# Optimization experiments

Measured on AMD Instinct MI355X. Metric: run time of the kernel, lower is better.

The kernel has to match this reference:

```python
import jax, jax.numpy as jnp
import numpy as np

IN_DIM = 512
C_OUT = IN_DIM // 8  # 64
B, H, W = 8, 128, 128


def setup_inputs() -> dict:
    key = jax.random.key(0)
    ks = jax.random.split(key, 6)
    x = jax.random.normal(ks[0], (B, IN_DIM, H, W), dtype=jnp.float32)
    # 1x1 conv weights stored as [out_ch, in_ch] matrices (kernel size 1)
    qkv_w = jax.random.normal(ks[1], (3 * C_OUT, IN_DIM), dtype=jnp.float32) * (1.0 / np.sqrt(IN_DIM))
    qkv_b = jax.random.normal(ks[2], (3 * C_OUT,), dtype=jnp.float32) * 0.01
    out_w = jax.random.normal(ks[3], (IN_DIM, C_OUT), dtype=jnp.float32) * (1.0 / np.sqrt(C_OUT))
    out_b = jax.random.normal(ks[4], (IN_DIM,), dtype=jnp.float32) * 0.01
    # gamma is init to 0 in torch; use a small nonzero value so both paths are exercised
    gamma = jnp.asarray(0.5, dtype=jnp.float32)
    return {"x": x, "qkv_w": qkv_w, "qkv_b": qkv_b, "out_w": out_w, "out_b": out_b, "gamma": gamma}


def reference(x, qkv_w, qkv_b, out_w, out_b, gamma):
    # qkv_conv: 1x1 conv == channel matmul
    qkv = jnp.einsum('bchw,oc->bohw', x, qkv_w) + qkv_b[None, :, None, None]
    q, k, v = jnp.split(qkv, 3, axis=1)  # each [B, C', H, W]

    # Horizontal branch: per column w, channel-channel attention contracting over H
    energy_h = jnp.einsum('bqhw,bkhw->bwqk', q, k)          # [B, W, C', C']
    attn_h = jax.nn.softmax(energy_h, axis=-1)
    out_h = jnp.einsum('bwqk,bkhw->bqhw', attn_h, v)        # [B, C', H, W]

    # Vertical branch: per row h, channel-channel attention contracting over W
    energy_v = jnp.einsum('bqhw,bkhw->bhqk', q, k)          # [B, H, C', C']
    attn_v = jax.nn.softmax(energy_v, axis=-1)
    out_v = jnp.einsum('bhqk,bkhw->bqhw', attn_v, v)        # [B, C', H, W]

    out = gamma * (out_h + out_v)
    out = jnp.einsum('bchw,oc->bohw', out, out_w) + out_b[None, :, None, None]
    return out + x
```

## Files before the change

kernel.cpp:

```cpp
#include <hip/hip_runtime.h>


typedef _Float16 f16;
typedef _Float16 f16x4 __attribute__((ext_vector_type(4)));
typedef _Float16 f16x8 __attribute__((ext_vector_type(8)));
typedef float f32x4 __attribute__((ext_vector_type(4)));

#define MFMA16(a, b, c) __builtin_amdgcn_mfma_f32_16x16x32_f16(a, b, c, 0, 0, 0)

constexpr int CIN = 512;
constexpr int COUT = 64;
constexpr int HW = 128;
constexpr int P = HW * HW;
constexpr int QKV_CH = 192;

__global__ __launch_bounds__(256) void qkv_gemm(
    const float* __restrict__ x, const float* __restrict__ w,
    const float* __restrict__ bias, f16* __restrict__ qkv)
{
  __shared__ __attribute__((aligned(16))) f16 Wl[QKV_CH * 40];
  __shared__ __attribute__((aligned(16))) f16 Xt[128 * 40];
  const int p0 = blockIdx.x * 128;
  const int b = blockIdx.y;
  const float* xb = x + (size_t)b * CIN * P;
  const int t = threadIdx.x;
  const int lane = t & 63, wv = t >> 6;
  const int quad = lane >> 4, l15 = lane & 15;
  const int wm = (wv >> 1) * 32, wn = (wv & 1) * 64;

  f32x4 acc[3][4][2] = {};
  for (int k0 = 0; k0 < CIN; k0 += 32) {
    for (int it = 0; it < 6; ++it) {
      int c = t + it * 256;
      int row = c >> 3, c4 = (c & 7) * 4;
      const float4 v = *(const float4*)(w + (size_t)row * CIN + k0 + c4);
      f16* d = &Wl[row * 40 + c4];
      d[0] = (f16)v.x; d[1] = (f16)v.y; d[2] = (f16)v.z; d[3] = (f16)v.w;
    }
    for (int it = 0; it < 4; ++it) {
      int c = t + it * 256;
      int kr = c >> 5, p4 = (c & 31) * 4;
      const float4 v = *(const float4*)(xb + (size_t)(k0 + kr) * P + p0 + p4);
      float vv[4] = {v.x, v.y, v.z, v.w};
#pragma unroll
      for (int j = 0; j < 4; ++j) {
        int p = p4 + j;
        int kc = kr ^ (((p >> 3) & 3) << 3);
        Xt[p * 40 + kc] = (f16)vv[j];
      }
    }
    __syncthreads();
    f16x8 xf[4];
#pragma unroll
    for (int ps = 0; ps < 4; ++ps) {
      int pr = wn + ps * 16 + l15;
      int kb = (quad * 8) ^ (((pr >> 3) & 3) << 3);
      xf[ps] = *(const f16x8*)&Xt[pr * 40 + kb];
    }
#pragma unroll
    for (int mt = 0; mt < 3; ++mt) {
      f16x8 wf[2];
#pragma unroll
      for (int ms = 0; ms < 2; ++ms)
        wf[ms] = *(const f16x8*)&Wl[(mt * 64 + wm + ms * 16 + l15) * 40 + quad * 8];
#pragma unroll
      for (int ps = 0; ps < 4; ++ps)
#pragma unroll
        for (int ms = 0; ms < 2; ++ms)
          acc[mt][ps][ms] = MFMA16(xf[ps], wf[ms], acc[mt][ps][ms]);
    }
    __syncthreads();
  }
  f16* ob = qkv + (size_t)b * QKV_CH * P;
#pragma unroll
  for (int mt = 0; mt < 3; ++mt) {
#pragma unroll
    for (int ms = 0; ms < 2; ++ms) {
      int m = mt * 64 + wm + ms * 16 + l15;
      float bi = bias[m];
#pragma unroll
      for (int ps = 0; ps < 4; ++ps) {
        int p = p0 + wn + ps * 16 + quad * 4;
        f16x4 tmp;
#pragma unroll
        for (int r = 0; r < 4; ++r) tmp[r] = (f16)(acc[mt][ps][ms][r] + bi);
        *(f16x4*)(ob + (size_t)m * P + p) = tmp;
      }
    }
  }
}

__global__ __launch_bounds__(256) void transpose_hw(
    const f16* __restrict__ in, f16* __restrict__ out)
{
  __shared__ __attribute__((aligned(16))) f16 T[64 * 72];
  const size_t plane = blockIdx.x;
  const int r0 = blockIdx.y * 64, c0 = blockIdx.z * 64;
  const f16* ip = in + plane * P;
  f16* op = out + plane * P;
  const int t = threadIdx.x;
  for (int it = 0; it < 2; ++it) {
    int c = t + it * 256;
    int row = c >> 3, c8 = (c & 7) * 8;
    *(f16x8*)&T[row * 72 + c8] =
        *(const f16x8*)(ip + (size_t)(r0 + row) * HW + c0 + c8);
  }
  __syncthreads();
  for (int it = 0; it < 2; ++it) {
    int c = t + it * 256;
    int wr = c >> 3, h8 = (c & 7) * 8;
    f16 tmp[8];
#pragma unroll
    for (int j = 0; j < 8; ++j) tmp[j] = T[(h8 + j) * 72 + wr];
    *(f16x8*)(op + (size_t)(c0 + wr) * HW + r0 + h8) = *(const f16x8*)tmp;
  }
}

__global__ __launch_bounds__(256) void cc_attn(
    const f16* __restrict__ qkvT, const f16* __restrict__ qkvN,
    f16* __restrict__ outT, f16* __restrict__ outN)
{
  __shared__ __attribute__((aligned(16))) f16 smem[64 * 136 * 2 + 128 * 72];
  f16* Ql = smem;
  f16* Kl = smem + 64 * 136;
  f16* Vt = smem + 2 * 64 * 136;
  f16* Al = smem;
  const int s = blockIdx.x, b = blockIdx.y;
  const f16* src = blockIdx.z ? qkvN : qkvT;
  f16* dst = blockIdx.z ? outN : outT;
  const f16* base = src + (size_t)b * QKV_CH * P + (size_t)s * HW;
  const int t = threadIdx.x;
  const int lane = t & 63, wv = t >> 6;
  const int quad = lane >> 4, l15 = lane & 15;

  for (int it = 0; it < 4; ++it) {
    int c = t + it * 256;
    int row = c >> 4, c8 = (c & 15) * 8;
    *(f16x8*)&Ql[row * 136 + c8] = *(const f16x8*)(base + (size_t)row * P + c8);
    *(f16x8*)&Kl[row * 136 + c8] =
        *(const f16x8*)(base + (size_t)(64 + row) * P + c8);
    f16x8 v = *(const f16x8*)(base + (size_t)(128 + row) * P + c8);
#pragma unroll
    for (int j = 0; j < 8; ++j) {
      int h = c8 + j;
      int kc = row ^ (((h >> 3) & 7) << 3);
      Vt[h * 72 + kc] = v[j];
    }
  }
  __syncthreads();

  const int m0 = wv * 16;
  f32x4 e[4] = {};
#pragma unroll
  for (int kk = 0; kk < 4; ++kk) {
    f16x8 aq = *(const f16x8*)&Ql[(m0 + l15) * 136 + kk * 32 + quad * 8];
#pragma unroll
    for (int nt = 0; nt < 4; ++nt) {
      f16x8 bk = *(const f16x8*)&Kl[(nt * 16 + l15) * 136 + kk * 32 + quad * 8];
      e[nt] = MFMA16(aq, bk, e[nt]);
    }
  }
  float pr[4][4];
  float rinv[4];
#pragma unroll
  for (int r = 0; r < 4; ++r) {
    float mx = fmaxf(fmaxf(e[0][r], e[1][r]), fmaxf(e[2][r], e[3][r]));
    for (int off = 1; off < 16; off <<= 1) mx = fmaxf(mx, __shfl_xor(mx, off));
    float sm = 0.f;
#pragma unroll
    for (int nt = 0; nt < 4; ++nt) {
      float pv = __expf(e[nt][r] - mx);
      pr[nt][r] = pv;
      sm += pv;
    }
    for (int off = 1; off < 16; off <<= 1) sm += __shfl_xor(sm, off);
    rinv[r] = 1.0f / sm;
  }
  __syncthreads();
#pragma unroll
  for (int nt = 0; nt < 4; ++nt)
#pragma unroll
    for (int r = 0; r < 4; ++r)
      Al[(m0 + quad * 4 + r) * 72 + nt * 16 + l15] = (f16)(pr[nt][r] * rinv[r]);
  __syncthreads();

  f32x4 o[8] = {};
#pragma unroll
  for (int kk = 0; kk < 2; ++kk) {
    f16x8 ap = *(const f16x8*)&Al[(m0 + l15) * 72 + kk * 32 + quad * 8];
#pragma unroll
    for (int nt = 0; nt < 8; ++nt) {
      int hr = nt * 16 + l15;
      int kb = (kk * 32 + quad * 8) ^ (((hr >> 3) & 7) << 3);
      f16x8 bv = *(const f16x8*)&Vt[hr * 72 + kb];
      o[nt] = MFMA16(ap, bv, o[nt]);
    }
  }
  f16* db = dst + (size_t)b * COUT * P + (size_t)s * HW;
#pragma unroll
  for (int nt = 0; nt < 8; ++nt)
#pragma unroll
    for (int r = 0; r < 4; ++r)
      db[(size_t)(m0 + quad * 4 + r) * P + nt * 16 + l15] = (f16)o[nt][r];
}

__global__ __launch_bounds__(256) void out_proj(
    const f16* __restrict__ ah, const f16* __restrict__ av,
    const float* __restrict__ w, const float* __restrict__ bias,
    const float* __restrict__ gamma_p, const float* __restrict__ x,
    float* __restrict__ out)
{
  __shared__ __attribute__((aligned(16))) f16 Wl[64 * 72];
  __shared__ __attribute__((aligned(16))) f16 St[128 * 72];
  const int m0 = blockIdx.x * 64;
  const int p0 = blockIdx.y * 128;
  const int b = blockIdx.z;
  const int t = threadIdx.x;
  const int lane = t & 63, wv = t >> 6;
  const int quad = lane >> 4, l15 = lane & 15;
  const int wm = (wv >> 1) * 32, wn = (wv & 1) * 64;

  for (int it = 0; it < 4; ++it) {
    int c = t + it * 256;
    int row = c >> 4, c4 = (c & 15) * 4;
    const float4 v = *(const float4*)(w + (size_t)(m0 + row) * COUT + c4);
    f16* d = &Wl[row * 72 + c4];
    d[0] = (f16)v.x; d[1] = (f16)v.y; d[2] = (f16)v.z; d[3] = (f16)v.w;
  }
  const size_t abase = (size_t)b * COUT * P + p0;
  for (int it = 0; it < 4; ++it) {
    int c = t + it * 256;
    int k = c >> 4, p8 = (c & 15) * 8;
    f16x8 a = *(const f16x8*)(ah + abase + (size_t)k * P + p8);
    f16x8 vv = *(const f16x8*)(av + abase + (size_t)k * P + p8);
#pragma unroll
    for (int j = 0; j < 8; ++j) {
      int p = p8 + j;
      int kc = k ^ (((p >> 3) & 7) << 3);
      St[p * 72 + kc] = (f16)(a[j] + vv[j]);
    }
  }
  __syncthreads();

  f32x4 acc[4][2] = {};
#pragma unroll
  for (int kk = 0; kk < 2; ++kk) {
    f16x8 sf[4], wf[2];
#pragma unroll
    for (int ps = 0; ps < 4; ++ps) {
      int pr2 = wn + ps * 16 + l15;
      int kb = (kk * 32 + quad * 8) ^ (((pr2 >> 3) & 7) << 3);
      sf[ps] = *(const f16x8*)&St[pr2 * 72 + kb];
    }
#pragma unroll
    for (int ms = 0; ms < 2; ++ms)
      wf[ms] = *(const f16x8*)&Wl[(wm + ms * 16 + l15) * 72 + kk * 32 + quad * 8];
#pragma unroll
    for (int ps = 0; ps < 4; ++ps)
#pragma unroll
      for (int ms = 0; ms < 2; ++ms)
        acc[ps][ms] = MFMA16(sf[ps], wf[ms], acc[ps][ms]);
  }
  const float g = *gamma_p;
  const float* xb = x + (size_t)b * CIN * P;
  float* ob = out + (size_t)b * CIN * P;
#pragma unroll
  for (int ms = 0; ms < 2; ++ms) {
    int m = m0 + wm + ms * 16 + l15;
    float bi = bias[m];
#pragma unroll
    for (int ps = 0; ps < 4; ++ps) {
      int p = p0 + wn + ps * 16 + quad * 4;
      size_t idx = (size_t)m * P + p;
      const float4 xv = *(const float4*)(xb + idx);
      float4 ov;
      ov.x = g * acc[ps][ms][0] + bi + xv.x;
      ov.y = g * acc[ps][ms][1] + bi + xv.y;
      ov.z = g * acc[ps][ms][2] + bi + xv.z;
      ov.w = g * acc[ps][ms][3] + bi + xv.w;
      *(float4*)(ob + idx) = ov;
    }
  }
}

extern "C" void kernel_launch(void* const* d_in, const int* in_sizes, int n_in,
                              void* d_out, int out_size, void* d_ws,
                              size_t ws_size, hipStream_t stream)
{
  (void)in_sizes; (void)n_in; (void)out_size; (void)ws_size;
  const float* x = (const float*)d_in[0];
  const float* qkv_w = (const float*)d_in[1];
  const float* qkv_b = (const float*)d_in[2];
  const float* out_w = (const float*)d_in[3];
  const float* out_b = (const float*)d_in[4];
  const float* gamma = (const float*)d_in[5];
  float* out = (float*)d_out;

  char* ws = (char*)d_ws;
  const size_t QKV_BYTES = (size_t)8 * QKV_CH * P * sizeof(f16);
  const size_t ATT_BYTES = (size_t)8 * COUT * P * sizeof(f16);
  f16* qkv  = (f16*)ws;
  f16* qkvT = (f16*)(ws + QKV_BYTES);
  f16* ahT  = (f16*)(ws + 2 * QKV_BYTES);
  f16* ahN  = (f16*)(ws + 2 * QKV_BYTES + ATT_BYTES);
  f16* avN  = (f16*)(ws + 2 * QKV_BYTES + 2 * ATT_BYTES);

  qkv_gemm<<<dim3(128, 8), 256, 0, stream>>>(x, qkv_w, qkv_b, qkv);
  transpose_hw<<<dim3(8 * QKV_CH, 2, 2), 256, 0, stream>>>(qkv, qkvT);
  cc_attn<<<dim3(128, 8, 2), 256, 0, stream>>>(qkvT, qkv, ahT, avN);
  transpose_hw<<<dim3(8 * COUT, 2, 2), 256, 0, stream>>>(ahT, ahN);
  out_proj<<<dim3(8, 128, 8), 256, 0, stream>>>(ahN, avN, out_w, out_b, gamma,
                                                x, out);
}
```

Measured before the change: 606.4 us.

## Reuse attention tile across all output channels and stage attention stores through LDS

```diff
diff --git a/kernel.cpp b/kernel.cpp
--- a/kernel.cpp
+++ b/kernel.cpp
@@ -116,15 +116,15 @@
   }
 }
 
-__global__ __launch_bounds__(256) void cc_attn(
+__global__ __launch_bounds__(256, 4) void cc_attn(
     const f16* __restrict__ qkvT, const f16* __restrict__ qkvN,
     f16* __restrict__ outT, f16* __restrict__ outN)
 {
-  __shared__ __attribute__((aligned(16))) f16 smem[64 * 136 * 2 + 128 * 72];
-  f16* Ql = smem;
-  f16* Kl = smem + 64 * 136;
-  f16* Vt = smem + 2 * 64 * 136;
+  __shared__ __attribute__((aligned(16))) f16 smem[64 * 136 + 128 * 72];
+  f16* Kl = smem;
+  f16* Vt = smem + 64 * 136;
   f16* Al = smem;
+  f16* Ol = smem;
   const int s = blockIdx.x, b = blockIdx.y;
   const f16* src = blockIdx.z ? qkvN : qkvT;
   f16* dst = blockIdx.z ? outN : outT;
@@ -132,11 +132,16 @@
   const int t = threadIdx.x;
   const int lane = t & 63, wv = t >> 6;
   const int quad = lane >> 4, l15 = lane & 15;
+  const int m0 = wv * 16;
+
+  f16x8 aq[4];
+#pragma unroll
+  for (int kk = 0; kk < 4; ++kk)
+    aq[kk] = *(const f16x8*)(base + (size_t)(m0 + l15) * P + kk * 32 + quad * 8);
 
   for (int it = 0; it < 4; ++it) {
     int c = t + it * 256;
     int row = c >> 4, c8 = (c & 15) * 8;
-    *(f16x8*)&Ql[row * 136 + c8] = *(const f16x8*)(base + (size_t)row * P + c8);
     *(f16x8*)&Kl[row * 136 + c8] =
         *(const f16x8*)(base + (size_t)(64 + row) * P + c8);
     f16x8 v = *(const f16x8*)(base + (size_t)(128 + row) * P + c8);
@@ -149,15 +154,13 @@
   }
   __syncthreads();
 
-  const int m0 = wv * 16;
   f32x4 e[4] = {};
 #pragma unroll
   for (int kk = 0; kk < 4; ++kk) {
-    f16x8 aq = *(const f16x8*)&Ql[(m0 + l15) * 136 + kk * 32 + quad * 8];
 #pragma unroll
     for (int nt = 0; nt < 4; ++nt) {
       f16x8 bk = *(const f16x8*)&Kl[(nt * 16 + l15) * 136 + kk * 32 + quad * 8];
-      e[nt] = MFMA16(aq, bk, e[nt]);
+      e[nt] = MFMA16(aq[kk], bk, e[nt]);
     }
   }
   float pr[4][4];
@@ -177,12 +180,12 @@
     rinv[r] = 1.0f / sm;
   }
   __syncthreads();
+
 #pragma unroll
   for (int nt = 0; nt < 4; ++nt)
 #pragma unroll
     for (int r = 0; r < 4; ++r)
       Al[(m0 + quad * 4 + r) * 72 + nt * 16 + l15] = (f16)(pr[nt][r] * rinv[r]);
-  __syncthreads();
 
   f32x4 o[8] = {};
 #pragma unroll
@@ -196,12 +199,25 @@
       o[nt] = MFMA16(ap, bv, o[nt]);
     }
   }
+  __syncthreads();
+
+#pragma unroll
+  for (int nt = 0; nt < 8; ++nt)
+#pragma unroll
+    for (int r = 0; r < 4; ++r) {
+      int row = m0 + quad * 4 + r;
+      int col = nt * 16 + l15;
+      Ol[row * 136 + (col ^ ((row & 15) << 3))] = (f16)o[nt][r];
+    }
   f16* db = dst + (size_t)b * COUT * P + (size_t)s * HW;
 #pragma unroll
-  for (int nt = 0; nt < 8; ++nt)
-#pragma unroll
-    for (int r = 0; r < 4; ++r)
-      db[(size_t)(m0 + quad * 4 + r) * P + nt * 16 + l15] = (f16)o[nt][r];
+  for (int it = 0; it < 4; ++it) {
+    int c = lane + it * 64;
+    int row = m0 + (c >> 4);
+    int c8 = (c & 15) * 8;
+    f16x8 vv = *(const f16x8*)&Ol[row * 136 + (c8 ^ ((row & 15) << 3))];
+    *(f16x8*)(db + (size_t)row * P + c8) = vv;
+  }
 }
 
 __global__ __launch_bounds__(256) void out_proj(
@@ -210,23 +226,14 @@
     const float* __restrict__ gamma_p, const float* __restrict__ x,
     float* __restrict__ out)
 {
-  __shared__ __attribute__((aligned(16))) f16 Wl[64 * 72];
   __shared__ __attribute__((aligned(16))) f16 St[128 * 72];
-  const int m0 = blockIdx.x * 64;
-  const int p0 = blockIdx.y * 128;
-  const int b = blockIdx.z;
+  const int p0 = blockIdx.x * 128;
+  const int b = blockIdx.y;
   const int t = threadIdx.x;
   const int lane = t & 63, wv = t >> 6;
   const int quad = lane >> 4, l15 = lane & 15;
   const int wm = (wv >> 1) * 32, wn = (wv & 1) * 64;
 
-  for (int it = 0; it < 4; ++it) {
-    int c = t + it * 256;
-    int row = c >> 4, c4 = (c & 15) * 4;
-    const float4 v = *(const float4*)(w + (size_t)(m0 + row) * COUT + c4);
-    f16* d = &Wl[row * 72 + c4];
-    d[0] = (f16)v.x; d[1] = (f16)v.y; d[2] = (f16)v.z; d[3] = (f16)v.w;
-  }
   const size_t abase = (size_t)b * COUT * P + p0;
   for (int it = 0; it < 4; ++it) {
     int c = t + it * 256;
@@ -242,43 +249,60 @@
   }
   __syncthreads();
 
-  f32x4 acc[4][2] = {};
-#pragma unroll
-  for (int kk = 0; kk < 2; ++kk) {
-    f16x8 sf[4], wf[2];
+  f16x8 sf[2][4];
+#pragma unroll
+  for (int kk = 0; kk < 2; ++kk)
 #pragma unroll
     for (int ps = 0; ps < 4; ++ps) {
       int pr2 = wn + ps * 16 + l15;
       int kb = (kk * 32 + quad * 8) ^ (((pr2 >> 3) & 7) << 3);
-      sf[ps] = *(const f16x8*)&St[pr2 * 72 + kb];
-    }
-#pragma unroll
-    for (int ms = 0; ms < 2; ++ms)
-      wf[ms] = *(const f16x8*)&Wl[(wm + ms * 16 + l15) * 72 + kk * 32 + quad * 8];
-#pragma unroll
-    for (int ps = 0; ps < 4; ++ps)
-#pragma unroll
-      for (int ms = 0; ms < 2; ++ms)
-        acc[ps][ms] = MFMA16(sf[ps], wf[ms], acc[ps][ms]);
-  }
+      sf[kk][ps] = *(const f16x8*)&St[pr2 * 72 + kb];
+    }
+
   const float g = *gamma_p;
   const float* xb = x + (size_t)b * CIN * P;
   float* ob = out + (size_t)b * CIN * P;
-#pragma unroll
-  for (int ms = 0; ms < 2; ++ms) {
-    int m = m0 + wm + ms * 16 + l15;
-    float bi = bias[m];
-#pragma unroll
-    for (int ps = 0; ps < 4; ++ps) {
-      int p = p0 + wn + ps * 16 + quad * 4;
-      size_t idx = (size_t)m * P + p;
-      const float4 xv = *(const float4*)(xb + idx);
-      float4 ov;
-      ov.x = g * acc[ps][ms][0] + bi + xv.x;
-      ov.y = g * acc[ps][ms][1] + bi + xv.y;
-      ov.z = g * acc[ps][ms][2] + bi + xv.z;
-      ov.w = g * acc[ps][ms][3] + bi + xv.w;
-      *(float4*)(ob + idx) = ov;
+
+  for (int mt = 0; mt < 8; ++mt) {
+    const int m0 = mt * 64;
+    f16x8 wf[2][2];
+#pragma unroll
+    for (int ms = 0; ms < 2; ++ms) {
+      const float* wr = w + (size_t)(m0 + wm + ms * 16 + l15) * COUT;
+#pragma unroll
+      for (int kk = 0; kk < 2; ++kk) {
+        const float4 w0 = *(const float4*)(wr + kk * 32 + quad * 8);
+        const float4 w1 = *(const float4*)(wr + kk * 32 + quad * 8 + 4);
+        f16x8 f;
+        f[0] = (f16)w0.x; f[1] = (f16)w0.y; f[2] = (f16)w0.z; f[3] = (f16)w0.w;
+        f[4] = (f16)w1.x; f[5] = (f16)w1.y; f[6] = (f16)w1.z; f[7] = (f16)w1.w;
+        wf[kk][ms] = f;
+      }
+    }
+    f32x4 acc[4][2] = {};
+#pragma unroll
+    for (int kk = 0; kk < 2; ++kk)
+#pragma unroll
+      for (int ps = 0; ps < 4; ++ps)
+#pragma unroll
+        for (int ms = 0; ms < 2; ++ms)
+          acc[ps][ms] = MFMA16(sf[kk][ps], wf[kk][ms], acc[ps][ms]);
+#pragma unroll
+    for (int ms = 0; ms < 2; ++ms) {
+      int m = m0 + wm + ms * 16 + l15;
+      float bi = bias[m];
+#pragma unroll
+      for (int ps = 0; ps < 4; ++ps) {
+        int p = p0 + wn + ps * 16 + quad * 4;
+        size_t idx = (size_t)m * P + p;
+        const float4 xv = *(const float4*)(xb + idx);
+        float4 ov;
+        ov.x = g * acc[ps][ms][0] + bi + xv.x;
+        ov.y = g * acc[ps][ms][1] + bi + xv.y;
+        ov.z = g * acc[ps][ms][2] + bi + xv.z;
+        ov.w = g * acc[ps][ms][3] + bi + xv.w;
+        *(float4*)(ob + idx) = ov;
+      }
     }
   }
 }
@@ -309,6 +333,6 @@
   transpose_hw<<<dim3(8 * QKV_CH, 2, 2), 256, 0, stream>>>(qkv, qkvT);
   cc_attn<<<dim3(128, 8, 2), 256, 0, stream>>>(qkvT, qkv, ahT, avN);
   transpose_hw<<<dim3(8 * COUT, 2, 2), 256, 0, stream>>>(ahT, ahN);
-  out_proj<<<dim3(8, 128, 8), 256, 0, stream>>>(ahN, avN, out_w, out_b, gamma,
-                                                x, out);
-}
+  out_proj<<<dim3(128, 8), 256, 0, stream>>>(ahN, avN, out_w, out_b, gamma,
+                                             x, out);
+}
```

Result: no change. 601.7 us (-0.8%).
